# Kernel tuning notes

Hardware: AMD Instinct MI355X
Metric: run time of the kernel (lower is better)

The kernel has to match this reference:

```python
import jax, jax.numpy as jnp
import numpy as np

N = 100000   # nodes
F = 32       # input features
D = 64       # dim_inner
E = 1600000  # edges
G = 2000     # graphs
C = 10       # classes
L = 4        # GIN layers
BN_EPS = 1e-5


def _bn(h, gamma, beta):
    # training-mode BatchNorm1d over node axis (biased variance, as torch)
    mu = jnp.mean(h, axis=0)
    var = jnp.mean((h - mu) ** 2, axis=0)
    return gamma * (h - mu) * jax.lax.rsqrt(var + BN_EPS) + beta


def setup_inputs() -> dict:
    key = jax.random.key(0)
    ks = jax.random.split(key, 24)
    s = 0.05
    f32 = jnp.float32
    x = jax.random.normal(ks[0], (N, F), f32)
    edge_index = jax.random.randint(ks[1], (2, E), 0, N)
    batch_ids = jnp.sort(jax.random.randint(ks[2], (N,), 0, G))
    y = jax.random.randint(ks[3], (G,), 0, C)
    W_enc = jax.random.normal(ks[4], (F, D), f32) * s
    b_enc = jnp.zeros((D,), f32)
    W1 = jax.random.normal(ks[5], (L, D, D), f32) * s
    b1 = jnp.zeros((L, D), f32)
    g1 = jnp.ones((L, D), f32)
    be1 = jnp.zeros((L, D), f32)
    W2 = jax.random.normal(ks[6], (L, D, D), f32) * s
    b2 = jnp.zeros((L, D), f32)
    gout = jnp.ones((L, D), f32)
    bout = jnp.zeros((L, D), f32)
    fcW0 = jax.random.normal(ks[7], (F, C), f32) * s
    fcb0 = jnp.zeros((C,), f32)
    fcW = jax.random.normal(ks[8], (L, D, C), f32) * s
    fcb = jnp.zeros((L, C), f32)
    return dict(x=x, edge_index=edge_index, batch_ids=batch_ids, y=y,
                W_enc=W_enc, b_enc=b_enc, W1=W1, b1=b1, g1=g1, be1=be1,
                W2=W2, b2=b2, gout=gout, bout=bout,
                fcW0=fcW0, fcb0=fcb0, fcW=fcW, fcb=fcb)


def reference(x, edge_index, batch_ids, y, W_enc, b_enc, W1, b1, g1, be1,
              W2, b2, gout, bout, fcW0, fcb0, fcW, fcb):
    src, dst = edge_index[0], edge_index[1]
    h = x @ W_enc + b_enc  # x_encoder
    layer_outs = []
    for i in range(L):
        # GINConv, eps=0: (1+eps)*x + sum_{j->i} x_j  (scatter-add over edges)
        agg = jax.ops.segment_sum(h[src], dst, num_segments=N)
        m = h + agg
        m = jax.nn.relu(_bn(m @ W1[i] + b1[i], g1[i], be1[i]))  # MLP part 1
        m = m @ W2[i] + b2[i]                                    # MLP part 2
        h = jax.nn.relu(_bn(m, gout[i], bout[i]))                # outer BN+ReLU
        layer_outs.append(h)
    # jumping-knowledge: pooled raw features + each layer through its fc head
    out = jax.ops.segment_sum(x, batch_ids, num_segments=G) @ fcW0 + fcb0
    for i in range(L):
        pooled = jax.ops.segment_sum(layer_outs[i], batch_ids, num_segments=G)
        out = out + pooled @ fcW[i] + fcb[i]
    return (out, y)
```

## Files before the change

kernel.cpp:

```cpp
#include <hip/hip_runtime.h>


#define BN_EPS 1e-5f
#define CURS_STRIDE 16

typedef __attribute__((ext_vector_type(8))) short short8;
typedef __attribute__((ext_vector_type(4))) float f32x4;

__device__ __forceinline__ unsigned int pack_bf16x2(float a, float b) {
    unsigned int ua = __float_as_uint(a);
    unsigned int ub = __float_as_uint(b);
    ua = (ua + 0x7FFFu + ((ua >> 16) & 1u)) >> 16;
    ub = (ub + 0x7FFFu + ((ub >> 16) & 1u)) >> 16;
    return ua | (ub << 16);
}
__device__ __forceinline__ unsigned short bf16_1(float f) {
    unsigned int u = __float_as_uint(f);
    u = (u + 0x7FFFu + ((u >> 16) & 1u)) >> 16;
    return (unsigned short)u;
}
__device__ __forceinline__ float2 unpack_bf16x2(unsigned int u) {
    float2 r;
    r.x = __uint_as_float(u << 16);
    r.y = __uint_as_float(u & 0xFFFF0000u);
    return r;
}

template<int K, int INK, bool STATS>
__global__ __launch_bounds__(256)
void mfma_gemm(const void* __restrict__ Av,
               const float* __restrict__ bn_sum, const float* __restrict__ bn_sumsq,
               const float* __restrict__ gamma, const float* __restrict__ beta,
               float invN,
               const float* __restrict__ W, const float* __restrict__ bias,
               unsigned short* __restrict__ out,
               float* __restrict__ stat_sum, float* __restrict__ stat_sumsq,
               int N)
{
    constexpr int AS  = K + 8;
    constexpr int WS  = K + 8;
    constexpr int CPR = K / 8;
    constexpr int KH  = K / 32;

    __shared__ short a_lds[128 * AS];
    __shared__ short wt_lds[64 * WS];
    __shared__ float ssf[128];
    __shared__ float red[512];

    const int tid = threadIdx.x;
    const int nb  = blockIdx.x * 128;
    const int l   = tid & 63;
    const int w   = tid >> 6;
    const int ln  = l & 15;
    const int q   = l >> 4;

    if (INK == 2) {
        if (tid < 64) {
            float mu  = bn_sum[tid] * invN;
            float var = bn_sumsq[tid] * invN - mu * mu;
            float s   = gamma[tid] * rsqrtf(var + BN_EPS);
            ssf[tid]      = s;
            ssf[64 + tid] = beta[tid] - s * mu;
        }
        __syncthreads();
    }

    for (int idx = tid; idx < K * 64; idx += 256) {
        int k = idx >> 6, n = idx & 63;
        wt_lds[n * WS + k] = (short)bf16_1(W[idx]);
    }

    for (int c = tid; c < 128 * CPR; c += 256) {
        int rloc = c / CPR;
        int j    = c % CPR;
        int row  = nb + rloc;
        uint4 p = make_uint4(0u, 0u, 0u, 0u);
        if (row < N) {
            if (INK == 1) {
                const float4* xr = (const float4*)Av;
                float4 f0 = xr[(size_t)row * (K / 4) + 2 * j];
                float4 f1 = xr[(size_t)row * (K / 4) + 2 * j + 1];
                p.x = pack_bf16x2(f0.x, f0.y); p.y = pack_bf16x2(f0.z, f0.w);
                p.z = pack_bf16x2(f1.x, f1.y); p.w = pack_bf16x2(f1.z, f1.w);
            } else {
                p = ((const uint4*)Av)[(size_t)row * CPR + j];
                if (INK == 2) {
                    int k0 = j * 8;
                    unsigned int* pp = (unsigned int*)&p;
                    #pragma unroll
                    for (int t = 0; t < 4; t++) {
                        float2 f = unpack_bf16x2(pp[t]);
                        int k = k0 + 2 * t;
                        f.x = fmaxf(fmaf(f.x, ssf[k],     ssf[64 + k]),     0.f);
                        f.y = fmaxf(fmaf(f.y, ssf[k + 1], ssf[64 + k + 1]), 0.f);
                        pp[t] = pack_bf16x2(f.x, f.y);
                    }
                }
            }
        }
        *(uint4*)&a_lds[rloc * AS + j * 8] = p;
    }
    __syncthreads();

    short8 afrag[2][KH], bfrag[4][KH];
    const int rw = w * 32;
    #pragma unroll
    for (int mt = 0; mt < 2; mt++)
        #pragma unroll
        for (int kh = 0; kh < KH; kh++)
            afrag[mt][kh] = *(const short8*)&a_lds[(rw + mt * 16 + ln) * AS + kh * 32 + q * 8];
    #pragma unroll
    for (int nt = 0; nt < 4; nt++)
        #pragma unroll
        for (int kh = 0; kh < KH; kh++)
            bfrag[nt][kh] = *(const short8*)&wt_lds[(nt * 16 + ln) * WS + kh * 32 + q * 8];

    f32x4 acc[2][4];
    #pragma unroll
    for (int nt = 0; nt < 4; nt++) {
        float bv = bias[nt * 16 + ln];
        #pragma unroll
        for (int mt = 0; mt < 2; mt++)
            acc[mt][nt] = (f32x4){bv, bv, bv, bv};
    }

    #pragma unroll
    for (int kh = 0; kh < KH; kh++)
        #pragma unroll
        for (int mt = 0; mt < 2; mt++)
            #pragma unroll
            for (int nt = 0; nt < 4; nt++)
                acc[mt][nt] = __builtin_amdgcn_mfma_f32_16x16x32_bf16(
                    afrag[mt][kh], bfrag[nt][kh], acc[mt][nt], 0, 0, 0);

    #pragma unroll
    for (int mt = 0; mt < 2; mt++) {
        #pragma unroll
        for (int reg = 0; reg < 4; reg++) {
            int row = nb + rw + mt * 16 + q * 4 + reg;
            if (row < N) {
                #pragma unroll
                for (int nt = 0; nt < 4; nt++)
                    out[(size_t)row * 64 + nt * 16 + ln] = bf16_1(acc[mt][nt][reg]);
            }
        }
    }

    if (STATS) {
        float s1[4] = {0.f, 0.f, 0.f, 0.f};
        float s2[4] = {0.f, 0.f, 0.f, 0.f};
        #pragma unroll
        for (int mt = 0; mt < 2; mt++) {
            #pragma unroll
            for (int reg = 0; reg < 4; reg++) {
                int row = nb + rw + mt * 16 + q * 4 + reg;
                if (row < N) {
                    #pragma unroll
                    for (int nt = 0; nt < 4; nt++) {
                        float v = acc[mt][nt][reg];
                        s1[nt] += v;
                        s2[nt] += v * v;
                    }
                }
            }
        }
        #pragma unroll
        for (int nt = 0; nt < 4; nt++) {
            s1[nt] += __shfl_xor(s1[nt], 16);
            s1[nt] += __shfl_xor(s1[nt], 32);
            s2[nt] += __shfl_xor(s2[nt], 16);
            s2[nt] += __shfl_xor(s2[nt], 32);
        }
        __syncthreads();
        if (ln == l) {}
        if (l < 16) {
            #pragma unroll
            for (int nt = 0; nt < 4; nt++) {
                red[w * 64 + nt * 16 + l]       = s1[nt];
                red[256 + w * 64 + nt * 16 + l] = s2[nt];
            }
        }
        __syncthreads();
        if (tid < 64) {
            float t1 = red[tid] + red[64 + tid] + red[128 + tid] + red[192 + tid];
            float t2 = red[256 + tid] + red[320 + tid] + red[384 + tid] + red[448 + tid];
            unsafeAtomicAdd(&stat_sum[tid],   t1);
            unsafeAtomicAdd(&stat_sumsq[tid], t2);
        }
    }
}

__global__ __launch_bounds__(256)
void bucket_hist(const int* __restrict__ dst, int* __restrict__ bhist,
                 int E, int nb)
{
    __shared__ int lh[1024];
    for (int i = threadIdx.x; i < 1024; i += 256) lh[i] = 0;
    __syncthreads();
    for (int e = blockIdx.x * 256 + threadIdx.x; e < E; e += gridDim.x * 256)
        atomicAdd(&lh[dst[e] >> 7], 1);
    __syncthreads();
    for (int i = threadIdx.x; i < nb; i += 256)
        if (lh[i]) atomicAdd(&bhist[i], lh[i]);
}

__global__ __launch_bounds__(1024)
void bucket_scan(const int* __restrict__ bhist, int* __restrict__ bbase,
                 int* __restrict__ bcur, int nb)
{
    __shared__ int sm[1024];
    int t = threadIdx.x;
    int v = (t < nb) ? bhist[t] : 0;
    sm[t] = v; __syncthreads();
    for (int off = 1; off < 1024; off <<= 1) {
        int add = (t >= off) ? sm[t - off] : 0;
        __syncthreads();
        sm[t] += add;
        __syncthreads();
    }
    if (t <= nb) {
        int ex = sm[t] - v;
        bbase[t] = ex;
        if (t < nb) bcur[t * CURS_STRIDE] = ex;
    }
}

__global__ __launch_bounds__(256)
void bucket_scatter(const int* __restrict__ src, const int* __restrict__ dst,
                    int* __restrict__ bcur, int* __restrict__ ebuf,
                    int E, int nb)
{
    constexpr int CH = 4096;
    __shared__ int            key[CH];
    __shared__ unsigned short bid[CH];
    __shared__ int lh[800];
    __shared__ int lbase[800];

    const int t    = threadIdx.x;
    const int base = blockIdx.x * CH;
    const int cnt  = min(CH, E - base);

    for (int i = t; i < nb; i += 256) lh[i] = 0;
    __syncthreads();

    for (int i = t; i < cnt; i += 256) {
        int d = dst[base + i];
        int s = src[base + i];
        int b = d >> 7;
        key[i] = (s << 7) | (d & 127);
        bid[i] = (unsigned short)b;
        atomicAdd(&lh[b], 1);
    }
    __syncthreads();

    for (int i = t; i < nb; i += 256) {
        int c = lh[i];
        if (c) lbase[i] = atomicAdd(&bcur[i * CURS_STRIDE], c);
        lh[i] = 0;
    }
    __syncthreads();

    for (int i = t; i < cnt; i += 256) {
        int b = bid[i];
        int p = atomicAdd(&lh[b], 1);
        ebuf[lbase[b] + p] = key[i];
    }
}

__global__ __launch_bounds__(256)
void bucket_csr(const int* __restrict__ bbase, const int* __restrict__ ebuf,
                int* __restrict__ row, int* __restrict__ srcs, int N, int E)
{
    __shared__ int lh[128], lofs[128], lcur[128];
    const int b   = blockIdx.x;
    const int tid = threadIdx.x;
    const int beg = bbase[b], end = bbase[b + 1];

    if (tid < 128) lh[tid] = 0;
    __syncthreads();
    for (int e = beg + tid; e < end; e += 256)
        atomicAdd(&lh[ebuf[e] & 127], 1);
    __syncthreads();

    int v = (tid < 128) ? lh[tid] : 0;
    if (tid < 128) lofs[tid] = v;
    __syncthreads();
    for (int off = 1; off < 128; off <<= 1) {
        int add = 0;
        if (tid < 128 && tid >= off) add = lofs[tid - off];
        __syncthreads();
        if (tid < 128) lofs[tid] += add;
        __syncthreads();
    }
    if (tid < 128) {
        int ex = lofs[tid] - v;
        lcur[tid] = ex;
        int node = b * 128 + tid;
        if (node < N) row[node] = beg + ex;
    }
    if (b == 0 && tid == 0) row[N] = E;
    __syncthreads();

    for (int e = beg + tid; e < end; e += 256) {
        int pk = ebuf[e];
        int p = atomicAdd(&lcur[pk & 127], 1);
        srcs[beg + p] = pk >> 7;
    }
}

template<bool BN>
__global__ __launch_bounds__(256)
void agg_gather(const int* __restrict__ row, const int* __restrict__ srcs,
                const unsigned int* __restrict__ hb,
                const float* __restrict__ bsum, const float* __restrict__ bsumsq,
                const float* __restrict__ gamma, const float* __restrict__ beta,
                float invN, unsigned int* __restrict__ m, int N)
{
    int tid = blockIdx.x * 256 + threadIdx.x;
    int n = tid >> 4;
    if (n >= N) return;
    int c4 = tid & 15;

    float4 s4 = make_float4(1.f, 1.f, 1.f, 1.f);
    float4 h4 = make_float4(0.f, 0.f, 0.f, 0.f);
    if (BN) {
        float4 su = ((const float4*)bsum)[c4];
        float4 sq = ((const float4*)bsumsq)[c4];
        float4 ga = ((const float4*)gamma)[c4];
        float4 be = ((const float4*)beta)[c4];
        float mx = su.x * invN, my = su.y * invN, mz = su.z * invN, mw = su.w * invN;
        s4.x = ga.x * rsqrtf(sq.x * invN - mx * mx + BN_EPS);
        s4.y = ga.y * rsqrtf(sq.y * invN - my * my + BN_EPS);
        s4.z = ga.z * rsqrtf(sq.z * invN - mz * mz + BN_EPS);
        s4.w = ga.w * rsqrtf(sq.w * invN - mw * mw + BN_EPS);
        h4.x = be.x - s4.x * mx; h4.y = be.y - s4.y * my;
        h4.z = be.z - s4.z * mz; h4.w = be.w - s4.w * mw;
    }
    const uint2* cur2 = (const uint2*)hb;

    float4 acc;
    {
        uint2 r = cur2[(size_t)n * 16 + c4];
        float2 lo = unpack_bf16x2(r.x), hi = unpack_bf16x2(r.y);
        acc.x = lo.x; acc.y = lo.y; acc.z = hi.x; acc.w = hi.y;
        if (BN) {
            acc.x = fmaxf(fmaf(acc.x, s4.x, h4.x), 0.f);
            acc.y = fmaxf(fmaf(acc.y, s4.y, h4.y), 0.f);
            acc.z = fmaxf(fmaf(acc.z, s4.z, h4.z), 0.f);
            acc.w = fmaxf(fmaf(acc.w, s4.w, h4.w), 0.f);
        }
    }

    int e = row[n], end = row[n + 1];
    for (; e + 3 < end; e += 4) {
        int a0 = srcs[e], a1 = srcs[e + 1], a2 = srcs[e + 2], a3 = srcs[e + 3];
        uint2 r0 = cur2[(size_t)a0 * 16 + c4];
        uint2 r1 = cur2[(size_t)a1 * 16 + c4];
        uint2 r2 = cur2[(size_t)a2 * 16 + c4];
        uint2 r3 = cur2[(size_t)a3 * 16 + c4];
        #pragma unroll
        for (int j = 0; j < 4; j++) {
            uint2 rr = (j == 0) ? r0 : (j == 1) ? r1 : (j == 2) ? r2 : r3;
            float2 lo = unpack_bf16x2(rr.x), hi = unpack_bf16x2(rr.y);
            float vx = lo.x, vy = lo.y, vz = hi.x, vw = hi.y;
            if (BN) {
                vx = fmaxf(fmaf(vx, s4.x, h4.x), 0.f);
                vy = fmaxf(fmaf(vy, s4.y, h4.y), 0.f);
                vz = fmaxf(fmaf(vz, s4.z, h4.z), 0.f);
                vw = fmaxf(fmaf(vw, s4.w, h4.w), 0.f);
            }
            acc.x += vx; acc.y += vy; acc.z += vz; acc.w += vw;
        }
    }
    for (; e < end; e++) {
        uint2 rr = cur2[(size_t)srcs[e] * 16 + c4];
        float2 lo = unpack_bf16x2(rr.x), hi = unpack_bf16x2(rr.y);
        float vx = lo.x, vy = lo.y, vz = hi.x, vw = hi.y;
        if (BN) {
            vx = fmaxf(fmaf(vx, s4.x, h4.x), 0.f);
            vy = fmaxf(fmaf(vy, s4.y, h4.y), 0.f);
            vz = fmaxf(fmaf(vz, s4.z, h4.z), 0.f);
            vw = fmaxf(fmaf(vw, s4.w, h4.w), 0.f);
        }
        acc.x += vx; acc.y += vy; acc.z += vz; acc.w += vw;
    }
    uint2 o;
    o.x = pack_bf16x2(acc.x, acc.y);
    o.y = pack_bf16x2(acc.z, acc.w);
    ((uint2*)m)[(size_t)n * 16 + c4] = o;
}

__global__ __launch_bounds__(256)
void pool_nodes(const unsigned short* __restrict__ hb,
                const float* __restrict__ bsum, const float* __restrict__ bsumsq,
                const float* __restrict__ gamma, const float* __restrict__ beta,
                float invN, const int* __restrict__ batch,
                float* __restrict__ pooled, int N)
{
    int d  = threadIdx.x & 63;
    int nl = threadIdx.x >> 6;
    int nb = blockIdx.x * 32;
    float mu  = bsum[d] * invN;
    float var = bsumsq[d] * invN - mu * mu;
    float s   = gamma[d] * rsqrtf(var + BN_EPS);
    float sh  = beta[d] - s * mu;
    float acc = 0.f;
    int cg = -1;
    #pragma unroll
    for (int r = 0; r < 8; r++) {
        int n = nb + nl * 8 + r;
        if (n >= N) break;
        int g = batch[n];
        if (g != cg) {
            if (cg >= 0) unsafeAtomicAdd(&pooled[(size_t)cg * 64 + d], acc);
            acc = 0.f; cg = g;
        }
        float v = __uint_as_float(((unsigned int)hb[(size_t)n * 64 + d]) << 16);
        acc += fmaxf(fmaf(v, s, sh), 0.f);
    }
    if (cg >= 0) unsafeAtomicAdd(&pooled[(size_t)cg * 64 + d], acc);
}

__global__ __launch_bounds__(256)
void pool_x(const float* __restrict__ x, const int* __restrict__ batch,
            float* __restrict__ px, int N)
{
    int f  = threadIdx.x & 31;
    int nl = threadIdx.x >> 5;
    int nb = blockIdx.x * 64;
    float acc = 0.f;
    int cg = -1;
    #pragma unroll
    for (int r = 0; r < 8; r++) {
        int n = nb + nl * 8 + r;
        if (n >= N) break;
        int g = batch[n];
        if (g != cg) {
            if (cg >= 0) unsafeAtomicAdd(&px[(size_t)cg * 32 + f], acc);
            acc = 0.f; cg = g;
        }
        acc += x[(size_t)n * 32 + f];
    }
    if (cg >= 0) unsafeAtomicAdd(&px[(size_t)cg * 32 + f], acc);
}

__global__ __launch_bounds__(256)
void head_kernel(const float* __restrict__ px, const float* __restrict__ pl,
                 const float* __restrict__ fcW0, const float* __restrict__ fcb0,
                 const float* __restrict__ fcW, const float* __restrict__ fcb,
                 const int* __restrict__ y, float* __restrict__ out, int G)
{
    int tid = blockIdx.x * 256 + threadIdx.x;
    int total = G * 10;
    if (tid < total) {
        int g = tid / 10, c = tid % 10;
        float acc = fcb0[c];
        const float* pxg = px + (size_t)g * 32;
        #pragma unroll
        for (int k = 0; k < 32; k++) acc = fmaf(pxg[k], fcW0[k * 10 + c], acc);
        #pragma unroll
        for (int i = 0; i < 4; i++) {
            acc += fcb[i * 10 + c];
            const float* pg = pl + ((size_t)i * G + g) * 64;
            const float* w  = fcW + i * 640;
            #pragma unroll
            for (int k = 0; k < 64; k++) acc = fmaf(pg[k], w[k * 10 + c], acc);
        }
        out[tid] = acc;
    } else if (tid < total + G) {
        out[tid] = (float)y[tid - total];
    }
}

extern "C" void kernel_launch(void* const* d_in, const int* in_sizes, int n_in,
                              void* d_out, int out_size, void* d_ws, size_t ws_size,
                              hipStream_t stream)
{
    const float* x     = (const float*)d_in[0];
    const int*   ei    = (const int*)  d_in[1];
    const int*   batch = (const int*)  d_in[2];
    const int*   y     = (const int*)  d_in[3];
    const float* W_enc = (const float*)d_in[4];
    const float* b_enc = (const float*)d_in[5];
    const float* W1    = (const float*)d_in[6];
    const float* b1    = (const float*)d_in[7];
    const float* g1    = (const float*)d_in[8];
    const float* be1   = (const float*)d_in[9];
    const float* W2    = (const float*)d_in[10];
    const float* b2    = (const float*)d_in[11];
    const float* gout  = (const float*)d_in[12];
    const float* bout  = (const float*)d_in[13];
    const float* fcW0  = (const float*)d_in[14];
    const float* fcb0  = (const float*)d_in[15];
    const float* fcW   = (const float*)d_in[16];
    const float* fcb   = (const float*)d_in[17];

    const int N = in_sizes[0] / 32;
    const int E = in_sizes[1] / 2;
    const int G = in_sizes[3];
    const int* src = ei;
    const int* dst = ei + E;
    const int NB = (N + 127) / 128;

    unsigned int* m  = (unsigned int*)d_ws;
    unsigned int* hb = m + (size_t)N * 32;
    float* stats = (float*)(hb + (size_t)N * 32);
    float* px    = stats + 1024;
    float* pl    = px + (size_t)G * 32;
    int*   row   = (int*)(pl + (size_t)4 * G * 64);
    int*   srcs  = row + (N + 1);
    int*   mi    = (int*)m;
    int*   bhist = mi;
    int*   bbase = mi + 1024;
    int*   bcur  = mi + 2048;
    int*   ebuf  = mi + 2048 + 800 * CURS_STRIDE;

    size_t zbytes = (size_t)(1024 + G * 32 + 4 * G * 64) * sizeof(float);
    hipMemsetAsync(stats, 0, zbytes, stream);
    hipMemsetAsync(bhist, 0, 1024 * sizeof(int), stream);

    bucket_hist<<<160, 256, 0, stream>>>(dst, bhist, E, NB);
    bucket_scan<<<1, 1024, 0, stream>>>(bhist, bbase, bcur, NB);
    bucket_scatter<<<(E + 4095) / 4096, 256, 0, stream>>>(src, dst, bcur, ebuf, E, NB);
    bucket_csr<<<NB, 256, 0, stream>>>(bbase, ebuf, row, srcs, N, E);

    const int gb = (N + 127) / 128;
    const float invN = 1.0f / (float)N;

    mfma_gemm<32, 1, false><<<gb, 256, 0, stream>>>(
        x, nullptr, nullptr, nullptr, nullptr, 0.f,
        W_enc, b_enc, (unsigned short*)hb, nullptr, nullptr, N);
    pool_x<<<(N + 63) / 64, 256, 0, stream>>>(x, batch, px, N);

    for (int i = 0; i < 4; i++) {
        float* s1a = stats + (i * 2 + 0) * 128;
        float* s1b = s1a + 64;
        float* s2a = stats + (i * 2 + 1) * 128;
        float* s2b = s2a + 64;

        if (i == 0) {
            agg_gather<false><<<(N * 16 + 255) / 256, 256, 0, stream>>>(
                row, srcs, hb, nullptr, nullptr, nullptr, nullptr, 0.f, m, N);
        } else {
            float* p2a = stats + ((i - 1) * 2 + 1) * 128;
            float* p2b = p2a + 64;
            agg_gather<true><<<(N * 16 + 255) / 256, 256, 0, stream>>>(
                row, srcs, hb, p2a, p2b,
                gout + (i - 1) * 64, bout + (i - 1) * 64, invN, m, N);
        }

        mfma_gemm<64, 0, true><<<gb, 256, 0, stream>>>(
            m, nullptr, nullptr, nullptr, nullptr, 0.f,
            W1 + (size_t)i * 4096, b1 + i * 64, (unsigned short*)m, s1a, s1b, N);

        mfma_gemm<64, 2, true><<<gb, 256, 0, stream>>>(
            m, s1a, s1b, g1 + i * 64, be1 + i * 64, invN,
            W2 + (size_t)i * 4096, b2 + i * 64, (unsigned short*)hb, s2a, s2b, N);

        pool_nodes<<<(N + 31) / 32, 256, 0, stream>>>(
            (const unsigned short*)hb, s2a, s2b, gout + i * 64, bout + i * 64, invN,
            batch, pl + (size_t)i * G * 64, N);
    }

    head_kernel<<<(G * 10 + G + 255) / 256, 256, 0, stream>>>(
        px, pl, fcW0, fcb0, fcW, fcb, y, (float*)d_out, G);
}
```

Measured before the change: 594.5 us.

## Fuse neighbor aggregation gather into first MLP GEMM kernel via LDS

Replaces the separate agg_gather kernel and the first mfma_gemm with a single gin_gemm1 kernel. Each 128-row block gathers neighbor rows (with the previous layer's BN+ReLU applied) into LDS, then runs the MFMA GEMM and BN statistics on them directly. This removes writing and re-reading the aggregated bf16 tensor through global memory and one launch per layer. In exchange the gather now uses 8 threads per node with 16-byte loads and far fewer blocks (one per 128 nodes), which may reduce memory-level parallelism for the latency-bound random gathers.

```diff
diff --git a/kernel.cpp b/kernel.cpp
--- a/kernel.cpp
+++ b/kernel.cpp
@@ -24,6 +24,189 @@
     r.x = __uint_as_float(u << 16);
     r.y = __uint_as_float(u & 0xFFFF0000u);
     return r;
+}
+
+template<bool BN>
+__device__ __forceinline__ void acc_row8(float (&acc)[8], uint4 p,
+                                         const float* sc, const float* sh) {
+    unsigned int pp[4] = {p.x, p.y, p.z, p.w};
+    #pragma unroll
+    for (int t = 0; t < 4; t++) {
+        float2 f = unpack_bf16x2(pp[t]);
+        if (BN) {
+            f.x = fmaxf(fmaf(f.x, sc[2 * t],     sh[2 * t]),     0.f);
+            f.y = fmaxf(fmaf(f.y, sc[2 * t + 1], sh[2 * t + 1]), 0.f);
+        }
+        acc[2 * t]     += f.x;
+        acc[2 * t + 1] += f.y;
+    }
+}
+
+template<bool BN>
+__global__ __launch_bounds__(256)
+void gin_gemm1(const int* __restrict__ rowp, const int* __restrict__ srcs,
+               const unsigned int* __restrict__ hb,
+               const float* __restrict__ bsum, const float* __restrict__ bsumsq,
+               const float* __restrict__ gamma, const float* __restrict__ beta,
+               float invN,
+               const float* __restrict__ W, const float* __restrict__ bias,
+               unsigned short* __restrict__ out,
+               float* __restrict__ stat_sum, float* __restrict__ stat_sumsq,
+               int N)
+{
+    constexpr int AS = 72, WS = 72, KH = 2;
+    __shared__ short a_lds[128 * AS];
+    __shared__ short wt_lds[64 * WS];
+    __shared__ float ssf[128];
+    __shared__ float red[512];
+
+    const int tid = threadIdx.x;
+    const int nb  = blockIdx.x * 128;
+    const int l   = tid & 63;
+    const int w   = tid >> 6;
+    const int ln  = l & 15;
+    const int q   = l >> 4;
+
+    if (BN) {
+        if (tid < 64) {
+            float mu  = bsum[tid] * invN;
+            float var = bsumsq[tid] * invN - mu * mu;
+            float s   = gamma[tid] * rsqrtf(var + BN_EPS);
+            ssf[tid]      = s;
+            ssf[64 + tid] = beta[tid] - s * mu;
+        }
+        __syncthreads();
+    }
+
+    for (int idx = tid; idx < 64 * 64; idx += 256) {
+        int k = idx >> 6, n = idx & 63;
+        wt_lds[n * WS + k] = (short)bf16_1(W[idx]);
+    }
+
+    const uint4* hb4 = (const uint4*)hb;
+    const int cc = tid & 7;
+    const int rl = tid >> 3;
+    float sc[8], sh[8];
+    if (BN) {
+        #pragma unroll
+        for (int j = 0; j < 8; j++) {
+            sc[j] = ssf[cc * 8 + j];
+            sh[j] = ssf[64 + cc * 8 + j];
+        }
+    }
+    for (int it = 0; it < 4; it++) {
+        int rloc = it * 32 + rl;
+        int n = nb + rloc;
+        float acc[8] = {0.f, 0.f, 0.f, 0.f, 0.f, 0.f, 0.f, 0.f};
+        if (n < N) {
+            uint4 p = hb4[(size_t)n * 8 + cc];
+            acc_row8<BN>(acc, p, sc, sh);
+            int e = rowp[n], end = rowp[n + 1];
+            for (; e + 3 < end; e += 4) {
+                int a0 = srcs[e], a1 = srcs[e + 1], a2 = srcs[e + 2], a3 = srcs[e + 3];
+                uint4 p0 = hb4[(size_t)a0 * 8 + cc];
+                uint4 p1 = hb4[(size_t)a1 * 8 + cc];
+                uint4 p2 = hb4[(size_t)a2 * 8 + cc];
+                uint4 p3 = hb4[(size_t)a3 * 8 + cc];
+                acc_row8<BN>(acc, p0, sc, sh);
+                acc_row8<BN>(acc, p1, sc, sh);
+                acc_row8<BN>(acc, p2, sc, sh);
+                acc_row8<BN>(acc, p3, sc, sh);
+            }
+            for (; e < end; e++) {
+                uint4 pp = hb4[(size_t)srcs[e] * 8 + cc];
+                acc_row8<BN>(acc, pp, sc, sh);
+            }
+        }
+        uint4 o;
+        o.x = pack_bf16x2(acc[0], acc[1]);
+        o.y = pack_bf16x2(acc[2], acc[3]);
+        o.z = pack_bf16x2(acc[4], acc[5]);
+        o.w = pack_bf16x2(acc[6], acc[7]);
+        *(uint4*)&a_lds[rloc * AS + cc * 8] = o;
+    }
+    __syncthreads();
+
+    short8 afrag[2][KH], bfrag[4][KH];
+    const int rw = w * 32;
+    #pragma unroll
+    for (int mt = 0; mt < 2; mt++)
+        #pragma unroll
+        for (int kh = 0; kh < KH; kh++)
+            afrag[mt][kh] = *(const short8*)&a_lds[(rw + mt * 16 + ln) * AS + kh * 32 + q * 8];
+    #pragma unroll
+    for (int nt = 0; nt < 4; nt++)
+        #pragma unroll
+        for (int kh = 0; kh < KH; kh++)
+            bfrag[nt][kh] = *(const short8*)&wt_lds[(nt * 16 + ln) * WS + kh * 32 + q * 8];
+
+    f32x4 acc[2][4];
+    #pragma unroll
+    for (int nt = 0; nt < 4; nt++) {
+        float bv = bias[nt * 16 + ln];
+        #pragma unroll
+        for (int mt = 0; mt < 2; mt++)
+            acc[mt][nt] = (f32x4){bv, bv, bv, bv};
+    }
+    #pragma unroll
+    for (int kh = 0; kh < KH; kh++)
+        #pragma unroll
+        for (int mt = 0; mt < 2; mt++)
+            #pragma unroll
+            for (int nt = 0; nt < 4; nt++)
+                acc[mt][nt] = __builtin_amdgcn_mfma_f32_16x16x32_bf16(
+                    afrag[mt][kh], bfrag[nt][kh], acc[mt][nt], 0, 0, 0);
+
+    #pragma unroll
+    for (int mt = 0; mt < 2; mt++)
+        #pragma unroll
+        for (int reg = 0; reg < 4; reg++) {
+            int row = nb + rw + mt * 16 + q * 4 + reg;
+            if (row < N)
+                #pragma unroll
+                for (int nt = 0; nt < 4; nt++)
+                    out[(size_t)row * 64 + nt * 16 + ln] = bf16_1(acc[mt][nt][reg]);
+        }
+
+    {
+        float s1[4] = {0.f, 0.f, 0.f, 0.f};
+        float s2[4] = {0.f, 0.f, 0.f, 0.f};
+        #pragma unroll
+        for (int mt = 0; mt < 2; mt++)
+            #pragma unroll
+            for (int reg = 0; reg < 4; reg++) {
+                int row = nb + rw + mt * 16 + q * 4 + reg;
+                if (row < N)
+                    #pragma unroll
+                    for (int nt = 0; nt < 4; nt++) {
+                        float v = acc[mt][nt][reg];
+                        s1[nt] += v;
+                        s2[nt] += v * v;
+                    }
+            }
+        #pragma unroll
+        for (int nt = 0; nt < 4; nt++) {
+            s1[nt] += __shfl_xor(s1[nt], 16);
+            s1[nt] += __shfl_xor(s1[nt], 32);
+            s2[nt] += __shfl_xor(s2[nt], 16);
+            s2[nt] += __shfl_xor(s2[nt], 32);
+        }
+        __syncthreads();
+        if (l < 16) {
+            #pragma unroll
+            for (int nt = 0; nt < 4; nt++) {
+                red[w * 64 + nt * 16 + l]       = s1[nt];
+                red[256 + w * 64 + nt * 16 + l] = s2[nt];
+            }
+        }
+        __syncthreads();
+        if (tid < 64) {
+            float t1 = red[tid] + red[64 + tid] + red[128 + tid] + red[192 + tid];
+            float t2 = red[256 + tid] + red[320 + tid] + red[384 + tid] + red[448 + tid];
+            unsafeAtomicAdd(&stat_sum[tid],   t1);
+            unsafeAtomicAdd(&stat_sumsq[tid], t2);
+        }
+    }
 }
 
 template<int K, int INK, bool STATS>
@@ -123,7 +306,6 @@
         for (int mt = 0; mt < 2; mt++)
             acc[mt][nt] = (f32x4){bv, bv, bv, bv};
     }
-
     #pragma unroll
     for (int kh = 0; kh < KH; kh++)
         #pragma unroll
@@ -134,36 +316,32 @@
                     afrag[mt][kh], bfrag[nt][kh], acc[mt][nt], 0, 0, 0);
 
     #pragma unroll
-    for (int mt = 0; mt < 2; mt++) {
+    for (int mt = 0; mt < 2; mt++)
         #pragma unroll
         for (int reg = 0; reg < 4; reg++) {
             int row = nb + rw + mt * 16 + q * 4 + reg;
-            if (row < N) {
+            if (row < N)
                 #pragma unroll
                 for (int nt = 0; nt < 4; nt++)
                     out[(size_t)row * 64 + nt * 16 + ln] = bf16_1(acc[mt][nt][reg]);
-            }
-        }
-    }
+        }
 
     if (STATS) {
         float s1[4] = {0.f, 0.f, 0.f, 0.f};
         float s2[4] = {0.f, 0.f, 0.f, 0.f};
         #pragma unroll
-        for (int mt = 0; mt < 2; mt++) {
+        for (int mt = 0; mt < 2; mt++)
             #pragma unroll
             for (int reg = 0; reg < 4; reg++) {
                 int row = nb + rw + mt * 16 + q * 4 + reg;
-                if (row < N) {
+                if (row < N)
                     #pragma unroll
                     for (int nt = 0; nt < 4; nt++) {
                         float v = acc[mt][nt][reg];
                         s1[nt] += v;
                         s2[nt] += v * v;
                     }
-                }
             }
-        }
         #pragma unroll
         for (int nt = 0; nt < 4; nt++) {
             s1[nt] += __shfl_xor(s1[nt], 16);
@@ -172,7 +350,6 @@
             s2[nt] += __shfl_xor(s2[nt], 32);
         }
         __syncthreads();
-        if (ln == l) {}
         if (l < 16) {
             #pragma unroll
             for (int nt = 0; nt < 4; nt++) {
@@ -306,88 +483,6 @@
         int p = atomicAdd(&lcur[pk & 127], 1);
         srcs[beg + p] = pk >> 7;
     }
-}
-
-template<bool BN>
-__global__ __launch_bounds__(256)
-void agg_gather(const int* __restrict__ row, const int* __restrict__ srcs,
-                const unsigned int* __restrict__ hb,
-                const float* __restrict__ bsum, const float* __restrict__ bsumsq,
-                const float* __restrict__ gamma, const float* __restrict__ beta,
-                float invN, unsigned int* __restrict__ m, int N)
-{
-    int tid = blockIdx.x * 256 + threadIdx.x;
-    int n = tid >> 4;
-    if (n >= N) return;
-    int c4 = tid & 15;
-
-    float4 s4 = make_float4(1.f, 1.f, 1.f, 1.f);
-    float4 h4 = make_float4(0.f, 0.f, 0.f, 0.f);
-    if (BN) {
-        float4 su = ((const float4*)bsum)[c4];
-        float4 sq = ((const float4*)bsumsq)[c4];
-        float4 ga = ((const float4*)gamma)[c4];
-        float4 be = ((const float4*)beta)[c4];
-        float mx = su.x * invN, my = su.y * invN, mz = su.z * invN, mw = su.w * invN;
-        s4.x = ga.x * rsqrtf(sq.x * invN - mx * mx + BN_EPS);
-        s4.y = ga.y * rsqrtf(sq.y * invN - my * my + BN_EPS);
-        s4.z = ga.z * rsqrtf(sq.z * invN - mz * mz + BN_EPS);
-        s4.w = ga.w * rsqrtf(sq.w * invN - mw * mw + BN_EPS);
-        h4.x = be.x - s4.x * mx; h4.y = be.y - s4.y * my;
-        h4.z = be.z - s4.z * mz; h4.w = be.w - s4.w * mw;
-    }
-    const uint2* cur2 = (const uint2*)hb;
-
-    float4 acc;
-    {
-        uint2 r = cur2[(size_t)n * 16 + c4];
-        float2 lo = unpack_bf16x2(r.x), hi = unpack_bf16x2(r.y);
-        acc.x = lo.x; acc.y = lo.y; acc.z = hi.x; acc.w = hi.y;
-        if (BN) {
-            acc.x = fmaxf(fmaf(acc.x, s4.x, h4.x), 0.f);
-            acc.y = fmaxf(fmaf(acc.y, s4.y, h4.y), 0.f);
-            acc.z = fmaxf(fmaf(acc.z, s4.z, h4.z), 0.f);
-            acc.w = fmaxf(fmaf(acc.w, s4.w, h4.w), 0.f);
-        }
-    }
-
-    int e = row[n], end = row[n + 1];
-    for (; e + 3 < end; e += 4) {
-        int a0 = srcs[e], a1 = srcs[e + 1], a2 = srcs[e + 2], a3 = srcs[e + 3];
-        uint2 r0 = cur2[(size_t)a0 * 16 + c4];
-        uint2 r1 = cur2[(size_t)a1 * 16 + c4];
-        uint2 r2 = cur2[(size_t)a2 * 16 + c4];
-        uint2 r3 = cur2[(size_t)a3 * 16 + c4];
-        #pragma unroll
-        for (int j = 0; j < 4; j++) {
-            uint2 rr = (j == 0) ? r0 : (j == 1) ? r1 : (j == 2) ? r2 : r3;
-            float2 lo = unpack_bf16x2(rr.x), hi = unpack_bf16x2(rr.y);
-            float vx = lo.x, vy = lo.y, vz = hi.x, vw = hi.y;
-            if (BN) {
-                vx = fmaxf(fmaf(vx, s4.x, h4.x), 0.f);
-                vy = fmaxf(fmaf(vy, s4.y, h4.y), 0.f);
-                vz = fmaxf(fmaf(vz, s4.z, h4.z), 0.f);
-                vw = fmaxf(fmaf(vw, s4.w, h4.w), 0.f);
-            }
-            acc.x += vx; acc.y += vy; acc.z += vz; acc.w += vw;
-        }
-    }
-    for (; e < end; e++) {
-        uint2 rr = cur2[(size_t)srcs[e] * 16 + c4];
-        float2 lo = unpack_bf16x2(rr.x), hi = unpack_bf16x2(rr.y);
-        float vx = lo.x, vy = lo.y, vz = hi.x, vw = hi.y;
-        if (BN) {
-            vx = fmaxf(fmaf(vx, s4.x, h4.x), 0.f);
-            vy = fmaxf(fmaf(vy, s4.y, h4.y), 0.f);
-            vz = fmaxf(fmaf(vz, s4.z, h4.z), 0.f);
-            vw = fmaxf(fmaf(vw, s4.w, h4.w), 0.f);
-        }
-        acc.x += vx; acc.y += vy; acc.z += vz; acc.w += vw;
-    }
-    uint2 o;
-    o.x = pack_bf16x2(acc.x, acc.y);
-    o.y = pack_bf16x2(acc.z, acc.w);
-    ((uint2*)m)[(size_t)n * 16 + c4] = o;
 }
 
 __global__ __launch_bounds__(256)
@@ -539,19 +634,17 @@
         float* s2b = s2a + 64;
 
         if (i == 0) {
-            agg_gather<false><<<(N * 16 + 255) / 256, 256, 0, stream>>>(
-                row, srcs, hb, nullptr, nullptr, nullptr, nullptr, 0.f, m, N);
+            gin_gemm1<false><<<gb, 256, 0, stream>>>(
+                row, srcs, hb, nullptr, nullptr, nullptr, nullptr, 0.f,
+                W1 + (size_t)i * 4096, b1 + i * 64, (unsigned short*)m, s1a, s1b, N);
         } else {
             float* p2a = stats + ((i - 1) * 2 + 1) * 128;
             float* p2b = p2a + 64;
-            agg_gather<true><<<(N * 16 + 255) / 256, 256, 0, stream>>>(
+            gin_gemm1<true><<<gb, 256, 0, stream>>>(
                 row, srcs, hb, p2a, p2b,
-                gout + (i - 1) * 64, bout + (i - 1) * 64, invN, m, N);
-        }
-
-        mfma_gemm<64, 0, true><<<gb, 256, 0, stream>>>(
-            m, nullptr, nullptr, nullptr, nullptr, 0.f,
-            W1 + (size_t)i * 4096, b1 + i * 64, (unsigned short*)m, s1a, s1b, N);
+                gout + (i - 1) * 64, bout + (i - 1) * 64, invN,
+                W1 + (size_t)i * 4096, b1 + i * 64, (unsigned short*)m, s1a, s1b, N);
+        }
 
         mfma_gemm<64, 2, true><<<gb, 256, 0, stream>>>(
             m, s1a, s1b, g1 + i * 64, be1 + i * 64, invN,
```

Result: faster. 564.6 us (-5.0%).
